# Kernel tuning notes

Measured on AMD Instinct MI355X. Metric: run time of the kernel, lower is better.

Reference implementation:

```python
import jax, jax.numpy as jnp
import numpy as np

B, N, DEG = 64, 512, 16        # graphs, nodes per graph, avg degree
C, HID = 10, 128               # input feat dim (== num_classes quirk), hidden
E = B * N * DEG                # total edges (fixed; pooling masks edges)


def _gcn(x, W, b, src, dst, emask, n):
    # PyG GCNConv: add self-loops, symmetric norm D^-1/2 (A+I) D^-1/2 (XW) + b
    h = x @ W
    deg = jax.ops.segment_sum(emask, dst, num_segments=n) + 1.0  # +1 self-loop
    dinv = jax.lax.rsqrt(deg)
    norm = dinv[src] * dinv[dst] * emask
    agg = jax.ops.segment_sum(h[src] * norm[:, None], dst, num_segments=n)
    return agg + h * (dinv * dinv)[:, None] + b  # self-loop term + bias


def _sag_pool(x, src, dst, emask, Wp, bp, n_per):
    # SAGPooling: score = tanh(GCN(x)); per-graph top-k (ratio=0.5); x' = x[perm]*score
    n = x.shape[0]
    score = jnp.tanh(_gcn(x, Wp, bp, src, dst, emask, n)[:, 0])
    k = n_per // 2
    vals, idx = jax.lax.top_k(score.reshape(B, n_per), k)  # [B,k]
    perm = (idx + (jnp.arange(B) * n_per)[:, None]).reshape(-1)
    xk = x[perm] * vals.reshape(-1)[:, None]
    # relabel edges; drop edges touching removed nodes via mask (fixed E)
    mapping = jnp.full((n,), -1, jnp.int32).at[perm].set(
        jnp.arange(B * k, dtype=jnp.int32))
    ns, nd = mapping[src], mapping[dst]
    nmask = emask * ((ns >= 0) & (nd >= 0)).astype(emask.dtype)
    return xk, jnp.maximum(ns, 0), jnp.maximum(nd, 0), nmask, k


def _readout(x, k):
    # global max pool || global mean pool (all kept nodes are real, no padding)
    xg = x.reshape(B, k, -1)
    return jnp.concatenate([xg.max(axis=1), xg.mean(axis=1)], axis=1)


def setup_inputs() -> dict:
    key = jax.random.key(0)
    ks = jax.random.split(key, 16)
    x = jax.random.normal(ks[0], (B * N, C), jnp.float32)
    off = jnp.repeat(jnp.arange(B, dtype=jnp.int32) * N, N * DEG)
    src = jax.random.randint(ks[1], (E,), 0, N, jnp.int32) + off
    dst = jax.random.randint(ks[2], (E,), 0, N, jnp.int32) + off
    p = lambda k, s: jax.random.normal(k, s, jnp.float32) * 0.05
    return {
        "x": x, "src": src, "dst": dst,
        "W1": p(ks[3], (C, HID)), "b1": jnp.zeros((HID,), jnp.float32),
        "W2": p(ks[4], (HID, HID)), "b2": jnp.zeros((HID,), jnp.float32),
        "W3": p(ks[5], (HID, HID)), "b3": jnp.zeros((HID,), jnp.float32),
        "Wp": p(ks[6], (HID, 1)), "bp": jnp.zeros((1,), jnp.float32),
        "L1W": p(ks[7], (2 * HID, HID)), "L1b": jnp.zeros((HID,), jnp.float32),
        "L2W": p(ks[8], (HID, HID // 2)), "L2b": jnp.zeros((HID // 2,), jnp.float32),
    }


def reference(x, src, dst, W1, b1, W2, b2, W3, b3, Wp, bp, L1W, L1b, L2W, L2b):
    emask = jnp.ones((E,), jnp.float32)
    h = jax.nn.relu(_gcn(x, W1, b1, src, dst, emask, B * N))
    h, src, dst, emask, k = _sag_pool(h, src, dst, emask, Wp, bp, N)
    x1 = _readout(h, k)
    h = jax.nn.relu(_gcn(h, W2, b2, src, dst, emask, B * k))
    h, src, dst, emask, k = _sag_pool(h, src, dst, emask, Wp, bp, k)
    x2 = _readout(h, k)
    h = jax.nn.relu(_gcn(h, W3, b3, src, dst, emask, B * k))
    h, src, dst, emask, k = _sag_pool(h, src, dst, emask, Wp, bp, k)
    x3 = _readout(h, k)
    z = x1 + x2 + x3
    z = jax.nn.relu(z @ L1W + L1b)
    # dropout inactive in eval mode
    z = jax.nn.relu(z @ L2W + L2b)
    return jax.nn.log_softmax(z, axis=1)
```

## Files before the change

### kernel.cpp

```cpp
#include <hip/hip_runtime.h>
#include <math.h>

#define BGR 64
#define N0 512
#define E_TOT (BGR*N0*16)
#define EPG 8192
#define EIT 16
#define HID 128


__global__ __launch_bounds__(512) void k_topo0(
    const int* __restrict__ s0, const int* __restrict__ d0,
    int2* __restrict__ edges, int* __restrict__ cnt, int* __restrict__ rowptr,
    float* __restrict__ dinv, int2* __restrict__ csr){
  __shared__ int   deg[512];
  __shared__ int   cur[512];
  __shared__ float dl[512];
  __shared__ int   wsum[8];
  int g = (blockIdx.x & 7)*8 + (blockIdx.x >> 3);
  int t = threadIdx.x;
  int gbase = g*N0, ebase = g*EPG;
  deg[t] = 0;
  __syncthreads();
  int2 ebuf[EIT];
  #pragma unroll
  for (int it = 0; it < EIT; it++){
    int i = ebase + it*512 + t;
    int2 e = make_int2(s0[i], d0[i]);
    ebuf[it] = e;
    edges[i] = e;
    atomicAdd(&deg[e.y - gbase], 1);
  }
  __syncthreads();
  int vdeg = deg[t];
  int lane = t & 63, wid = t >> 6;
  int x = vdeg;
  #pragma unroll
  for (int off = 1; off < 64; off <<= 1){
    int y = __shfl_up(x, off);
    if (lane >= off) x += y;
  }
  if (lane == 63) wsum[wid] = x;
  __syncthreads();
  int prefix = 0;
  #pragma unroll
  for (int wj = 0; wj < 8; wj++) prefix += (wj < wid) ? wsum[wj] : 0;
  int excl = x + prefix - vdeg;
  rowptr[gbase + t] = ebase + excl;
  cnt[gbase + t] = vdeg;
  cur[t] = excl;
  float dv = rsqrtf((float)vdeg + 1.f);
  dl[t] = dv;
  dinv[gbase + t] = dv;
  __syncthreads();
  #pragma unroll
  for (int it = 0; it < EIT; it++){
    int2 e = ebuf[it];
    int sl = e.x - gbase, dc = e.y - gbase;
    int pos = atomicAdd(&cur[dc], 1);
    csr[ebase + pos] = make_int2(e.x, __float_as_int(dl[sl]*dl[dc]));
  }
}

__global__ __launch_bounds__(512) void k_l1_fused(
    const float* __restrict__ x, const float* __restrict__ W1,
    const int2* __restrict__ csr, const int* __restrict__ rowptr,
    const int* __restrict__ cnt, const float* __restrict__ dinv,
    const float* __restrict__ b1, const float* __restrict__ Wp,
    float4* __restrict__ gout4, float* __restrict__ hp_part){
  extern __shared__ float hl[];
  int b = blockIdx.x;
  int xcd = b & 7, idx = b >> 3;
  int graph = xcd*8 + (idx >> 3);
  int sub = idx & 7;
  int qf = sub >> 1, half = sub & 1;
  int t = threadIdx.x;
  int gbase = graph*N0;
  int fp = t & 31;
  int f = qf*32 + fp;
  float wcol[10];
  #pragma unroll
  for (int k = 0; k < 10; k++) wcol[k] = W1[k*HID + f];
  for (int n = t >> 5; n < N0; n += 16){
    const float* xr = x + (gbase + n)*10;
    float acc = 0.f;
    #pragma unroll
    for (int k = 0; k < 10; k++) acc += xr[k]*wcol[k];
    hl[n*32 + fp] = acc;
  }
  __syncthreads();
  const float4* hl4 = (const float4*)hl;
  int l = t & 7, grp = t >> 3;
  float4 bb = ((const float4*)b1)[qf*8 + l];
  float4 wp = ((const float4*)Wp)[qf*8 + l];
  int n0 = half*256;
  for (int nl = n0 + grp; nl < n0 + 256; nl += 64){
    int node = gbase + nl;
    int start = rowptr[node], c = cnt[node];
    float4 acc = make_float4(0.f,0.f,0.f,0.f);
    int j = 0;
    for (; j + 4 <= c; j += 4){
      int2 e0 = csr[start+j],   e1 = csr[start+j+1];
      int2 e2 = csr[start+j+2], e3 = csr[start+j+3];
      float4 h0 = hl4[(e0.x - gbase)*8 + l];
      float4 h1 = hl4[(e1.x - gbase)*8 + l];
      float4 h2 = hl4[(e2.x - gbase)*8 + l];
      float4 h3 = hl4[(e3.x - gbase)*8 + l];
      float w0 = __int_as_float(e0.y), w1 = __int_as_float(e1.y);
      float w2 = __int_as_float(e2.y), w3 = __int_as_float(e3.y);
      acc.x += w0*h0.x + w1*h1.x + w2*h2.x + w3*h3.x;
      acc.y += w0*h0.y + w1*h1.y + w2*h2.y + w3*h3.y;
      acc.z += w0*h0.z + w1*h1.z + w2*h2.z + w3*h3.z;
      acc.w += w0*h0.w + w1*h1.w + w2*h2.w + w3*h3.w;
    }
    for (; j < c; j++){
      int2 e = csr[start + j];
      float wgt = __int_as_float(e.y);
      float4 hv = hl4[(e.x - gbase)*8 + l];
      acc.x += wgt*hv.x; acc.y += wgt*hv.y; acc.z += wgt*hv.z; acc.w += wgt*hv.w;
    }
    float di = dinv[node], dd = di*di;
    float4 hs = hl4[nl*8 + l];
    float4 v;
    v.x = fmaxf(acc.x + hs.x*dd + bb.x, 0.f);
    v.y = fmaxf(acc.y + hs.y*dd + bb.y, 0.f);
    v.z = fmaxf(acc.z + hs.z*dd + bb.z, 0.f);
    v.w = fmaxf(acc.w + hs.w*dd + bb.w, 0.f);
    gout4[node*32 + qf*8 + l] = v;
    float contrib = v.x*wp.x + v.y*wp.y + v.z*wp.z + v.w*wp.w;
    #pragma unroll
    for (int off = 4; off; off >>= 1) contrib += __shfl_down(contrib, off, 8);
    if (l == 0) hp_part[qf*32768 + node] = contrib;
  }
}

__global__ void k_gemm16p(const float* __restrict__ gprev,
                          const int* __restrict__ sig,
                          const float* __restrict__ svg,
                          const float* __restrict__ W,
                          float* __restrict__ out, int nprev, int nper){
  __shared__ float xr[16][HID];
  int b = blockIdx.x;
  int xcd = b & 7, idx = b >> 3, bpg = nper >> 4;
  int graph = xcd*8 + idx / bpg;
  int lb = (idx % bpg)*16;
  int f = threadIdx.x;
  #pragma unroll
  for (int nd = 0; nd < 16; nd++){
    int row  = sig[graph*512 + lb + nd];
    float val = svg[graph*512 + lb + nd];
    xr[nd][f] = gprev[(graph*nprev + row)*HID + f] * val;
  }
  __syncthreads();
  float acc[16];
  #pragma unroll
  for (int nd = 0; nd < 16; nd++) acc[nd] = 0.f;
  for (int i = 0; i < HID; i++){
    float wv = W[i*HID + f];
    #pragma unroll
    for (int nd = 0; nd < 16; nd++) acc[nd] += xr[nd][i]*wv;
  }
  #pragma unroll
  for (int nd = 0; nd < 16; nd++) out[(graph*nper + lb + nd)*HID + f] = acc[nd];
}

__global__ __launch_bounds__(256) void k_gcn_gather(
    const float4* __restrict__ h4, const int2* __restrict__ csr,
    const int* __restrict__ rowptr, const int* __restrict__ cnt,
    const float* __restrict__ dinv, const float4* __restrict__ bias4,
    const float4* __restrict__ Wp4, float4* __restrict__ out4,
    float* __restrict__ hp, int nper){
  int b = blockIdx.x;
  int xcd = b & 7, idx = b >> 3, bpg = nper >> 3;
  int graph = xcd*8 + idx / bpg;
  int node = graph*nper + (idx % bpg)*8 + (threadIdx.x >> 5);
  int l = threadIdx.x & 31;
  int start = rowptr[node], c = cnt[node];
  float4 acc = make_float4(0.f, 0.f, 0.f, 0.f);
  int j = 0;
  for (; j + 4 <= c; j += 4){
    int2 e0 = csr[start+j],   e1 = csr[start+j+1];
    int2 e2 = csr[start+j+2], e3 = csr[start+j+3];
    float4 h0 = h4[e0.x*32 + l];
    float4 h1 = h4[e1.x*32 + l];
    float4 h2 = h4[e2.x*32 + l];
    float4 h3 = h4[e3.x*32 + l];
    float w0 = __int_as_float(e0.y), w1 = __int_as_float(e1.y);
    float w2 = __int_as_float(e2.y), w3 = __int_as_float(e3.y);
    acc.x += w0*h0.x + w1*h1.x + w2*h2.x + w3*h3.x;
    acc.y += w0*h0.y + w1*h1.y + w2*h2.y + w3*h3.y;
    acc.z += w0*h0.z + w1*h1.z + w2*h2.z + w3*h3.z;
    acc.w += w0*h0.w + w1*h1.w + w2*h2.w + w3*h3.w;
  }
  for (; j < c; j++){
    int2 e = csr[start + j];
    float wgt = __int_as_float(e.y);
    float4 hv = h4[e.x*32 + l];
    acc.x += wgt*hv.x; acc.y += wgt*hv.y; acc.z += wgt*hv.z; acc.w += wgt*hv.w;
  }
  float di = dinv[node], dd = di*di;
  float4 hs = h4[node*32 + l];
  float4 bb = bias4[l];
  float4 v;
  v.x = fmaxf(acc.x + hs.x*dd + bb.x, 0.f);
  v.y = fmaxf(acc.y + hs.y*dd + bb.y, 0.f);
  v.z = fmaxf(acc.z + hs.z*dd + bb.z, 0.f);
  v.w = fmaxf(acc.w + hs.w*dd + bb.w, 0.f);
  out4[node*32 + l] = v;
  float4 wp = Wp4[l];
  float contrib = v.x*wp.x + v.y*wp.y + v.z*wp.z + v.w*wp.w;
  #pragma unroll
  for (int off = 16; off; off >>= 1) contrib += __shfl_down(contrib, off, 32);
  if (l == 0) hp[node] = contrib;
}

__global__ __launch_bounds__(1024) void k_mega(
    const float4* __restrict__ gout4, const float* __restrict__ hp_part,
    int l1flag, const float* __restrict__ hp,
    int2* __restrict__ csr, int* __restrict__ rowptr, int* __restrict__ cnt,
    float* __restrict__ dinv, const float* __restrict__ bp,
    int2* __restrict__ edges, int* __restrict__ sig, float* __restrict__ svg,
    float* __restrict__ z, int nper, int lastlev,
    const float* __restrict__ L1W, const float* __restrict__ L1b,
    const float* __restrict__ L2W, const float* __restrict__ L2b,
    float* __restrict__ out){
  __shared__ float sv[512];
  __shared__ int   si[512];
  __shared__ float hpl[512];
  __shared__ float spart[1024];
  __shared__ int   map_[512];
  __shared__ int   sb[512];
  __shared__ int   cur[256];
  __shared__ float dl[256];
  __shared__ int   wsum[4];
  __shared__ float4 pmx[16][32];
  __shared__ float4 psm[16][32];
  __shared__ float zr[256];
  __shared__ float h1[128];
  __shared__ float h2[64];
  __shared__ float red[2];
  int g = (blockIdx.x & 7)*8 + (blockIdx.x >> 3);
  int t = threadIdx.x;
  int k = nper >> 1;
  int gbase = g*nper, ebase = g*EPG, gb2 = g*k;
  int SPL = 1024/nper;
  int n = t & (nper-1), p = t / nper;
  bool act = t < nper;

  if (act){
    int node = gbase + t;
    hpl[t] = l1flag ? (hp_part[node] + hp_part[32768 + node] +
                       hp_part[65536 + node] + hp_part[98304 + node])
                    : hp[node];
  }
  __syncthreads();
  {
    int start = rowptr[gbase + n], c = cnt[gbase + n];
    int lo = (c*p)/SPL, hi = (c*(p+1))/SPL;
    float a = 0.f;
    for (int j = lo; j < hi; j++){
      int2 e = csr[start + j];
      a += __int_as_float(e.y)*hpl[e.x - gbase];
    }
    spart[t] = a;
  }
  __syncthreads();
  float v = 0.f; int idx = t;
  if (act){
    float a = 0.f;
    for (int pp = 0; pp < SPL; pp++) a += spart[t + pp*nper];
    float di = dinv[gbase + t];
    v = tanhf(a + hpl[t]*di*di + bp[0]);
  }
  for (int kk = 2; kk <= nper; kk <<= 1){
    for (int jj = kk >> 1; jj > 0; jj >>= 1){
      if (jj >= 64){
        if (act){ sv[t] = v; si[t] = idx; }
        __syncthreads();
        if (act){
          int pr = t ^ jj;
          float pv = sv[pr]; int pi = si[pr];
          bool amLower = (t & jj) == 0;
          bool dirDesc = (t & kk) == 0;
          bool betterMine = (v > pv) || (v == pv && idx < pi);
          if ((amLower == dirDesc) != betterMine){ v = pv; idx = pi; }
        }
        __syncthreads();
      } else if (act){
        float pv = __shfl_xor(v, jj);
        int   pi = __shfl_xor(idx, jj);
        bool amLower = (t & jj) == 0;
        bool dirDesc = (t & kk) == 0;
        bool betterMine = (v > pv) || (v == pv && idx < pi);
        if ((amLower == dirDesc) != betterMine){ v = pv; idx = pi; }
      }
    }
  }
  if (act){ sv[t] = v; si[t] = idx; }
  __syncthreads();
  int l = t & 31, j0 = t >> 5;
  if (t < 512){
    float4 mx = make_float4(-INFINITY,-INFINITY,-INFINITY,-INFINITY);
    float4 sm = make_float4(0.f,0.f,0.f,0.f);
    for (int j = j0; j < k; j += 16){
      float val = sv[j]; int row = si[j];
      float4 hv = gout4[(gbase + row)*32 + l];
      float4 o = make_float4(hv.x*val, hv.y*val, hv.z*val, hv.w*val);
      mx.x = fmaxf(mx.x, o.x); mx.y = fmaxf(mx.y, o.y);
      mx.z = fmaxf(mx.z, o.z); mx.w = fmaxf(mx.w, o.w);
      sm.x += o.x; sm.y += o.y; sm.z += o.z; sm.w += o.w;
    }
    pmx[j0][l] = mx; psm[j0][l] = sm;
  }
  if (t < 512 && t < k && !lastlev){ sig[g*512 + t] = si[t]; svg[g*512 + t] = sv[t]; }
  __syncthreads();
  if (t < 32){
    float4 M = pmx[0][t], S = psm[0][t];
    #pragma unroll
    for (int q = 1; q < 16; q++){
      float4 m2 = pmx[q][t], s2 = psm[q][t];
      M.x = fmaxf(M.x, m2.x); M.y = fmaxf(M.y, m2.y);
      M.z = fmaxf(M.z, m2.z); M.w = fmaxf(M.w, m2.w);
      S.x += s2.x; S.y += s2.y; S.z += s2.z; S.w += s2.w;
    }
    float ki = 1.f/(float)k;
    float* zp = z + g*256;
    if (l1flag){
      zp[t*4+0] = M.x; zp[t*4+1] = M.y; zp[t*4+2] = M.z; zp[t*4+3] = M.w;
      zp[128+t*4+0] = S.x*ki; zp[128+t*4+1] = S.y*ki;
      zp[128+t*4+2] = S.z*ki; zp[128+t*4+3] = S.w*ki;
    } else if (!lastlev){
      zp[t*4+0] += M.x; zp[t*4+1] += M.y; zp[t*4+2] += M.z; zp[t*4+3] += M.w;
      zp[128+t*4+0] += S.x*ki; zp[128+t*4+1] += S.y*ki;
      zp[128+t*4+2] += S.z*ki; zp[128+t*4+3] += S.w*ki;
    } else {
      zr[t*4+0] = zp[t*4+0] + M.x; zr[t*4+1] = zp[t*4+1] + M.y;
      zr[t*4+2] = zp[t*4+2] + M.z; zr[t*4+3] = zp[t*4+3] + M.w;
      zr[128+t*4+0] = zp[128+t*4+0] + S.x*ki;
      zr[128+t*4+1] = zp[128+t*4+1] + S.y*ki;
      zr[128+t*4+2] = zp[128+t*4+2] + S.z*ki;
      zr[128+t*4+3] = zp[128+t*4+3] + S.w*ki;
    }
  }
  if (lastlev){
    __syncthreads();
    if (t < 128){
      float a = L1b[t];
      for (int i = 0; i < 256; i++) a += zr[i]*L1W[i*128 + t];
      h1[t] = fmaxf(a, 0.f);
    }
    __syncthreads();
    if (t < 64){
      float a = L2b[t];
      for (int i = 0; i < 128; i++) a += h1[i]*L2W[i*64 + t];
      h2[t] = fmaxf(a, 0.f);
    }
    __syncthreads();
    if (t == 0){
      float mxv = -INFINITY;
      for (int i = 0; i < 64; i++) mxv = fmaxf(mxv, h2[i]);
      float s = 0.f;
      for (int i = 0; i < 64; i++) s += expf(h2[i] - mxv);
      red[0] = mxv; red[1] = logf(s);
    }
    __syncthreads();
    if (t < 64) out[g*64 + t] = h2[t] - red[0] - red[1];
    return;
  }
  if (act) map_[t] = -1;
  if (t < k) sb[t] = 0;
  __syncthreads();
  if (t < k) map_[si[t]] = t;
  __syncthreads();
  int2 ebuf[8];
  #pragma unroll
  for (int it = 0; it < 8; it++){
    int i = ebase + it*1024 + t;
    int2 e = edges[i];
    int2 ne = make_int2(-1, 0);
    if (e.x >= 0){
      int ns = map_[e.x - gbase], nd = map_[e.y - gbase];
      if (ns >= 0 && nd >= 0){
        ne = make_int2(gb2 + ns, gb2 + nd);
        atomicAdd(&sb[nd], 1);
      }
    }
    ebuf[it] = ne;
    edges[i] = ne;
  }
  __syncthreads();
  int vdeg = (t < k) ? sb[t] : 0;
  int lane = t & 63, wid = t >> 6;
  int x = vdeg;
  #pragma unroll
  for (int off = 1; off < 64; off <<= 1){
    int y = __shfl_up(x, off);
    if (lane >= off) x += y;
  }
  if (t < k && lane == 63) wsum[wid] = x;
  __syncthreads();
  if (t < k){
    int prefix = 0;
    #pragma unroll
    for (int wj = 0; wj < 4; wj++) prefix += (wj < wid) ? wsum[wj] : 0;
    int excl = x + prefix - vdeg;
    rowptr[gb2 + t] = ebase + excl;
    cnt[gb2 + t] = vdeg;
    cur[t] = excl;
    float dv = rsqrtf((float)vdeg + 1.f);
    dl[t] = dv;
    dinv[gb2 + t] = dv;
  }
  __syncthreads();
  #pragma unroll
  for (int it = 0; it < 8; it++){
    int2 e = ebuf[it];
    if (e.x >= 0){
      int sl = e.x - gb2, dc = e.y - gb2;
      int pos = atomicAdd(&cur[dc], 1);
      csr[ebase + pos] = make_int2(e.x, __float_as_int(dl[sl]*dl[dc]));
    }
  }
}

extern "C" void kernel_launch(void* const* d_in, const int* in_sizes, int n_in,
                              void* d_out, int out_size, void* d_ws, size_t ws_size,
                              hipStream_t stream){
  (void)in_sizes; (void)n_in; (void)out_size; (void)ws_size;
  const float* x0  = (const float*)d_in[0];
  const int*   s0  = (const int*)  d_in[1];
  const int*   d0  = (const int*)  d_in[2];
  const float* W1  = (const float*)d_in[3];  const float* b1 = (const float*)d_in[4];
  const float* W2  = (const float*)d_in[5];  const float* b2 = (const float*)d_in[6];
  const float* W3  = (const float*)d_in[7];  const float* b3 = (const float*)d_in[8];
  const float* Wp  = (const float*)d_in[9];  const float* bp = (const float*)d_in[10];
  const float* L1W = (const float*)d_in[11]; const float* L1b = (const float*)d_in[12];
  const float* L2W = (const float*)d_in[13]; const float* L2b = (const float*)d_in[14];
  float* out = (float*)d_out;

  float* w = (float*)d_ws;
  float* h     = w; w += 32768*HID;
  float* gout  = w; w += 32768*HID;
  float* dinvv = w; w += 32768;
  float* hp    = w; w += 32768;
  float* hppt  = w; w += 4*32768;
  float* z     = w; w += BGR*256;
  float* svg   = w; w += 32768;
  int* sig     = (int*)w; w += 32768;
  int* cnt     = (int*)w; w += 32768;
  int* rowptr  = (int*)w; w += 32768;
  int2* edges  = (int2*)w; w += 2*E_TOT;
  int2* csr    = (int2*)w; w += 2*E_TOT;

  k_topo0<<<BGR, 512, 0, stream>>>(s0, d0, edges, cnt, rowptr, dinvv, csr);

  k_l1_fused<<<512, 512, 65536, stream>>>(x0, W1, csr, rowptr, cnt, dinvv,
                                          b1, Wp, (float4*)gout, hppt);
  k_mega<<<BGR, 1024, 0, stream>>>((const float4*)gout, hppt, 1, hp, csr,
                                   rowptr, cnt, dinvv, bp, edges, sig, svg,
                                   z, 512, 0, L1W, L1b, L2W, L2b, out);
  k_gemm16p<<<16384/16, HID, 0, stream>>>(gout, sig, svg, W2, h, 512, 256);
  k_gcn_gather<<<16384/8, 256, 0, stream>>>((const float4*)h, csr, rowptr, cnt,
                                            dinvv, (const float4*)b2,
                                            (const float4*)Wp, (float4*)gout,
                                            hp, 256);
  k_mega<<<BGR, 1024, 0, stream>>>((const float4*)gout, hppt, 0, hp, csr,
                                   rowptr, cnt, dinvv, bp, edges, sig, svg,
                                   z, 256, 0, L1W, L1b, L2W, L2b, out);
  k_gemm16p<<<8192/16, HID, 0, stream>>>(gout, sig, svg, W3, h, 256, 128);
  k_gcn_gather<<<8192/8, 256, 0, stream>>>((const float4*)h, csr, rowptr, cnt,
                                           dinvv, (const float4*)b3,
                                           (const float4*)Wp, (float4*)gout,
                                           hp, 128);
  k_mega<<<BGR, 1024, 0, stream>>>((const float4*)gout, hppt, 0, hp, csr,
                                   rowptr, cnt, dinvv, bp, edges, sig, svg,
                                   z, 128, 1, L1W, L1b, L2W, L2b, out);
}
```

Before: 243.0 us.

## Fuse pooling, GEMM and GCN gather into per-level per-graph mega kernels

Replaces the generic mega kernel plus separate gemm16p and gcn_gather launches with three specialized per-graph kernels (megaA/B/C). Each one fuses pooling, the next layer's weight GEMM and the GCN gather into a single 1024-thread block per graph, keeping features in LDS and using per-level CSR offsets. This cuts the launch count from nine to five and removes global round trips. It also swizzles the LDS layout in the layer-1 kernel to reduce bank conflicts. In exchange, each level now runs on only 64 blocks, so parallelism for the GEMM and gather drops sharply.

```diff
diff --git a/kernel.cpp b/kernel.cpp
--- a/kernel.cpp
+++ b/kernel.cpp
@@ -7,7 +7,102 @@
 #define EPG 8192
 #define EIT 16
 #define HID 128
-
+#define LOFF2 32768
+#define LOFF3 49152
+
+#define HSW(r,l) (((r)<<3) | (((l)+(r))&7))
+
+__device__ __forceinline__ void bitonic_sort(float* sv, int* si, float v, int idx,
+                                             int t, int nper, bool act){
+  for (int kk = 2; kk <= nper; kk <<= 1){
+    for (int jj = kk >> 1; jj > 0; jj >>= 1){
+      if (jj >= 64){
+        if (act){ sv[t] = v; si[t] = idx; }
+        __syncthreads();
+        if (act){
+          int p = t ^ jj;
+          float pv = sv[p]; int pi = si[p];
+          bool amLower = (t & jj) == 0;
+          bool dirDesc = (t & kk) == 0;
+          bool betterMine = (v > pv) || (v == pv && idx < pi);
+          if ((amLower == dirDesc) != betterMine){ v = pv; idx = pi; }
+        }
+        __syncthreads();
+      } else if (act){
+        float pv = __shfl_xor(v, jj);
+        int   pi = __shfl_xor(idx, jj);
+        bool amLower = (t & jj) == 0;
+        bool dirDesc = (t & kk) == 0;
+        bool betterMine = (v > pv) || (v == pv && idx < pi);
+        if ((amLower == dirDesc) != betterMine){ v = pv; idx = pi; }
+      }
+    }
+  }
+  if (act){ sv[t] = v; si[t] = idx; }
+  __syncthreads();
+}
+
+__device__ __forceinline__ void relabel1024(
+    int2* __restrict__ edges, int2* __restrict__ csr, const int* si,
+    int* map_, int* sb, int* cur, float* dl, int* wsum,
+    int* __restrict__ rowptr, int* __restrict__ cnt, float* __restrict__ dinv,
+    int t, int nper, int k, int gbase, int gbnew, int ebase, int loff){
+  if (t < nper) map_[t] = -1;
+  if (t < k) sb[t] = 0;
+  __syncthreads();
+  if (t < k) map_[si[t]] = t;
+  __syncthreads();
+  int2 ebuf[8];
+  #pragma unroll
+  for (int it = 0; it < 8; it++){
+    int i = ebase + it*1024 + t;
+    int2 e = edges[i];
+    int2 ne = make_int2(-1, 0);
+    if (e.x >= 0){
+      int ns = map_[e.x - gbase], nd = map_[e.y - gbase];
+      if (ns >= 0 && nd >= 0){
+        ne = make_int2(gbnew + ns, gbnew + nd);
+        atomicAdd(&sb[nd], 1);
+      }
+    }
+    ebuf[it] = ne;
+    edges[i] = ne;
+  }
+  __syncthreads();
+  int vdeg = (t < k) ? sb[t] : 0;
+  int lane = t & 63, wid = t >> 6;
+  int x = vdeg;
+  #pragma unroll
+  for (int off = 1; off < 64; off <<= 1){
+    int y = __shfl_up(x, off);
+    if (lane >= off) x += y;
+  }
+  if (t < k && lane == 63) wsum[wid] = x;
+  __syncthreads();
+  if (t < k){
+    int prefix = 0;
+    #pragma unroll
+    for (int wj = 0; wj < 4; wj++) prefix += (wj < wid) ? wsum[wj] : 0;
+    int excl = x + prefix - vdeg;
+    rowptr[loff + gbnew + t] = ebase + excl;
+    cnt[loff + gbnew + t] = vdeg;
+    cur[t] = excl;
+    float dv = rsqrtf((float)vdeg + 1.f);
+    dl[t] = dv;
+    dinv[loff + gbnew + t] = dv;
+  }
+  __syncthreads();
+  #pragma unroll
+  for (int it = 0; it < 8; it++){
+    int2 e = ebuf[it];
+    if (e.x >= 0){
+      int sl = e.x - gbnew, dc = e.y - gbnew;
+      int pos = atomicAdd(&cur[dc], 1);
+      csr[ebase + pos] = make_int2(e.x, __float_as_int(dl[sl]*dl[dc]));
+    }
+  }
+  __syncthreads();
+}
 
 __global__ __launch_bounds__(512) void k_topo0(
     const int* __restrict__ s0, const int* __restrict__ d0,
@@ -86,7 +181,7 @@
     float acc = 0.f;
     #pragma unroll
     for (int k = 0; k < 10; k++) acc += xr[k]*wcol[k];
-    hl[n*32 + fp] = acc;
+    hl[n*32 + ((((fp>>2)+n)&7)<<2) + (fp&3)] = acc;
   }
   __syncthreads();
   const float4* hl4 = (const float4*)hl;
@@ -102,10 +197,10 @@
     for (; j + 4 <= c; j += 4){
       int2 e0 = csr[start+j],   e1 = csr[start+j+1];
       int2 e2 = csr[start+j+2], e3 = csr[start+j+3];
-      float4 h0 = hl4[(e0.x - gbase)*8 + l];
-      float4 h1 = hl4[(e1.x - gbase)*8 + l];
-      float4 h2 = hl4[(e2.x - gbase)*8 + l];
-      float4 h3 = hl4[(e3.x - gbase)*8 + l];
+      float4 h0 = hl4[HSW(e0.x - gbase, l)];
+      float4 h1 = hl4[HSW(e1.x - gbase, l)];
+      float4 h2 = hl4[HSW(e2.x - gbase, l)];
+      float4 h3 = hl4[HSW(e3.x - gbase, l)];
       float w0 = __int_as_float(e0.y), w1 = __int_as_float(e1.y);
       float w2 = __int_as_float(e2.y), w3 = __int_as_float(e3.y);
       acc.x += w0*h0.x + w1*h1.x + w2*h2.x + w3*h3.x;
@@ -116,11 +211,11 @@
     for (; j < c; j++){
       int2 e = csr[start + j];
       float wgt = __int_as_float(e.y);
-      float4 hv = hl4[(e.x - gbase)*8 + l];
+      float4 hv = hl4[HSW(e.x - gbase, l)];
       acc.x += wgt*hv.x; acc.y += wgt*hv.y; acc.z += wgt*hv.z; acc.w += wgt*hv.w;
     }
     float di = dinv[node], dd = di*di;
-    float4 hs = hl4[nl*8 + l];
+    float4 hs = hl4[HSW(nl, l)];
     float4 v;
     v.x = fmaxf(acc.x + hs.x*dd + bb.x, 0.f);
     v.y = fmaxf(acc.y + hs.y*dd + bb.y, 0.f);
@@ -134,175 +229,57 @@
   }
 }
 
-__global__ void k_gemm16p(const float* __restrict__ gprev,
-                          const int* __restrict__ sig,
-                          const float* __restrict__ svg,
-                          const float* __restrict__ W,
-                          float* __restrict__ out, int nprev, int nper){
-  __shared__ float xr[16][HID];
-  int b = blockIdx.x;
-  int xcd = b & 7, idx = b >> 3, bpg = nper >> 4;
-  int graph = xcd*8 + idx / bpg;
-  int lb = (idx % bpg)*16;
-  int f = threadIdx.x;
-  #pragma unroll
-  for (int nd = 0; nd < 16; nd++){
-    int row  = sig[graph*512 + lb + nd];
-    float val = svg[graph*512 + lb + nd];
-    xr[nd][f] = gprev[(graph*nprev + row)*HID + f] * val;
-  }
-  __syncthreads();
-  float acc[16];
-  #pragma unroll
-  for (int nd = 0; nd < 16; nd++) acc[nd] = 0.f;
-  for (int i = 0; i < HID; i++){
-    float wv = W[i*HID + f];
-    #pragma unroll
-    for (int nd = 0; nd < 16; nd++) acc[nd] += xr[nd][i]*wv;
-  }
-  #pragma unroll
-  for (int nd = 0; nd < 16; nd++) out[(graph*nper + lb + nd)*HID + f] = acc[nd];
-}
-
-__global__ __launch_bounds__(256) void k_gcn_gather(
-    const float4* __restrict__ h4, const int2* __restrict__ csr,
-    const int* __restrict__ rowptr, const int* __restrict__ cnt,
-    const float* __restrict__ dinv, const float4* __restrict__ bias4,
-    const float4* __restrict__ Wp4, float4* __restrict__ out4,
-    float* __restrict__ hp, int nper){
-  int b = blockIdx.x;
-  int xcd = b & 7, idx = b >> 3, bpg = nper >> 3;
-  int graph = xcd*8 + idx / bpg;
-  int node = graph*nper + (idx % bpg)*8 + (threadIdx.x >> 5);
-  int l = threadIdx.x & 31;
-  int start = rowptr[node], c = cnt[node];
-  float4 acc = make_float4(0.f, 0.f, 0.f, 0.f);
-  int j = 0;
-  for (; j + 4 <= c; j += 4){
-    int2 e0 = csr[start+j],   e1 = csr[start+j+1];
-    int2 e2 = csr[start+j+2], e3 = csr[start+j+3];
-    float4 h0 = h4[e0.x*32 + l];
-    float4 h1 = h4[e1.x*32 + l];
-    float4 h2 = h4[e2.x*32 + l];
-    float4 h3 = h4[e3.x*32 + l];
-    float w0 = __int_as_float(e0.y), w1 = __int_as_float(e1.y);
-    float w2 = __int_as_float(e2.y), w3 = __int_as_float(e3.y);
-    acc.x += w0*h0.x + w1*h1.x + w2*h2.x + w3*h3.x;
-    acc.y += w0*h0.y + w1*h1.y + w2*h2.y + w3*h3.y;
-    acc.z += w0*h0.z + w1*h1.z + w2*h2.z + w3*h3.z;
-    acc.w += w0*h0.w + w1*h1.w + w2*h2.w + w3*h3.w;
-  }
-  for (; j < c; j++){
-    int2 e = csr[start + j];
-    float wgt = __int_as_float(e.y);
-    float4 hv = h4[e.x*32 + l];
-    acc.x += wgt*hv.x; acc.y += wgt*hv.y; acc.z += wgt*hv.z; acc.w += wgt*hv.w;
-  }
-  float di = dinv[node], dd = di*di;
-  float4 hs = h4[node*32 + l];
-  float4 bb = bias4[l];
-  float4 v;
-  v.x = fmaxf(acc.x + hs.x*dd + bb.x, 0.f);
-  v.y = fmaxf(acc.y + hs.y*dd + bb.y, 0.f);
-  v.z = fmaxf(acc.z + hs.z*dd + bb.z, 0.f);
-  v.w = fmaxf(acc.w + hs.w*dd + bb.w, 0.f);
-  out4[node*32 + l] = v;
-  float4 wp = Wp4[l];
-  float contrib = v.x*wp.x + v.y*wp.y + v.z*wp.z + v.w*wp.w;
-  #pragma unroll
-  for (int off = 16; off; off >>= 1) contrib += __shfl_down(contrib, off, 32);
-  if (l == 0) hp[node] = contrib;
-}
-
-__global__ __launch_bounds__(1024) void k_mega(
-    const float4* __restrict__ gout4, const float* __restrict__ hp_part,
-    int l1flag, const float* __restrict__ hp,
+__global__ __launch_bounds__(1024) void k_megaA(
+    const float4* __restrict__ gout4, const float* __restrict__ hppt,
     int2* __restrict__ csr, int* __restrict__ rowptr, int* __restrict__ cnt,
     float* __restrict__ dinv, const float* __restrict__ bp,
-    int2* __restrict__ edges, int* __restrict__ sig, float* __restrict__ svg,
-    float* __restrict__ z, int nper, int lastlev,
-    const float* __restrict__ L1W, const float* __restrict__ L1b,
-    const float* __restrict__ L2W, const float* __restrict__ L2b,
-    float* __restrict__ out){
+    int2* __restrict__ edges, const float* __restrict__ W2,
+    float* __restrict__ h2, float* __restrict__ z){
   __shared__ float sv[512];
   __shared__ int   si[512];
   __shared__ float hpl[512];
-  __shared__ float spart[1024];
-  __shared__ int   map_[512];
-  __shared__ int   sb[512];
-  __shared__ int   cur[256];
+  __shared__ union UA {
+    float spart[1024];
+    struct { float4 pmx[16][32]; float4 psm[16][32]; } ro;
+    struct { int map_[512]; int sb[512]; int cur[256]; } rl;
+  } u;
   __shared__ float dl[256];
   __shared__ int   wsum[4];
-  __shared__ float4 pmx[16][32];
-  __shared__ float4 psm[16][32];
-  __shared__ float zr[256];
-  __shared__ float h1[128];
-  __shared__ float h2[64];
-  __shared__ float red[2];
+  __shared__ float xch[64*HID];
   int g = (blockIdx.x & 7)*8 + (blockIdx.x >> 3);
   int t = threadIdx.x;
-  int k = nper >> 1;
-  int gbase = g*nper, ebase = g*EPG, gb2 = g*k;
-  int SPL = 1024/nper;
-  int n = t & (nper-1), p = t / nper;
-  bool act = t < nper;
-
-  if (act){
+  int gbase = g*N0, ebase = g*EPG, gb2 = g*256;
+  float bp0 = bp[0];
+  if (t < 512){
     int node = gbase + t;
-    hpl[t] = l1flag ? (hp_part[node] + hp_part[32768 + node] +
-                       hp_part[65536 + node] + hp_part[98304 + node])
-                    : hp[node];
+    hpl[t] = hppt[node] + hppt[32768+node] + hppt[65536+node] + hppt[98304+node];
   }
   __syncthreads();
   {
+    int n = t & 511, p = t >> 9;
     int start = rowptr[gbase + n], c = cnt[gbase + n];
-    int lo = (c*p)/SPL, hi = (c*(p+1))/SPL;
+    int lo = (c*p) >> 1, hi = (c*(p+1)) >> 1;
     float a = 0.f;
     for (int j = lo; j < hi; j++){
       int2 e = csr[start + j];
       a += __int_as_float(e.y)*hpl[e.x - gbase];
     }
-    spart[t] = a;
+    u.spart[t] = a;
   }
   __syncthreads();
   float v = 0.f; int idx = t;
-  if (act){
-    float a = 0.f;
-    for (int pp = 0; pp < SPL; pp++) a += spart[t + pp*nper];
+  if (t < 512){
+    float a = u.spart[t] + u.spart[t + 512];
     float di = dinv[gbase + t];
-    v = tanhf(a + hpl[t]*di*di + bp[0]);
-  }
-  for (int kk = 2; kk <= nper; kk <<= 1){
-    for (int jj = kk >> 1; jj > 0; jj >>= 1){
-      if (jj >= 64){
-        if (act){ sv[t] = v; si[t] = idx; }
-        __syncthreads();
-        if (act){
-          int pr = t ^ jj;
-          float pv = sv[pr]; int pi = si[pr];
-          bool amLower = (t & jj) == 0;
-          bool dirDesc = (t & kk) == 0;
-          bool betterMine = (v > pv) || (v == pv && idx < pi);
-          if ((amLower == dirDesc) != betterMine){ v = pv; idx = pi; }
-        }
-        __syncthreads();
-      } else if (act){
-        float pv = __shfl_xor(v, jj);
-        int   pi = __shfl_xor(idx, jj);
-        bool amLower = (t & jj) == 0;
-        bool dirDesc = (t & kk) == 0;
-        bool betterMine = (v > pv) || (v == pv && idx < pi);
-        if ((amLower == dirDesc) != betterMine){ v = pv; idx = pi; }
-      }
-    }
-  }
-  if (act){ sv[t] = v; si[t] = idx; }
-  __syncthreads();
+    v = tanhf(a + hpl[t]*di*di + bp0);
+  }
+  __syncthreads();
+  bitonic_sort(sv, si, v, idx, t, 512, t < 512);
   int l = t & 31, j0 = t >> 5;
   if (t < 512){
     float4 mx = make_float4(-INFINITY,-INFINITY,-INFINITY,-INFINITY);
     float4 sm = make_float4(0.f,0.f,0.f,0.f);
-    for (int j = j0; j < k; j += 16){
+    for (int j = j0; j < 256; j += 16){
       float val = sv[j]; int row = si[j];
       float4 hv = gout4[(gbase + row)*32 + l];
       float4 o = make_float4(hv.x*val, hv.y*val, hv.z*val, hv.w*val);
@@ -310,117 +287,348 @@
       mx.z = fmaxf(mx.z, o.z); mx.w = fmaxf(mx.w, o.w);
       sm.x += o.x; sm.y += o.y; sm.z += o.z; sm.w += o.w;
     }
-    pmx[j0][l] = mx; psm[j0][l] = sm;
-  }
-  if (t < 512 && t < k && !lastlev){ sig[g*512 + t] = si[t]; svg[g*512 + t] = sv[t]; }
+    u.ro.pmx[j0][l] = mx; u.ro.psm[j0][l] = sm;
+  }
   __syncthreads();
   if (t < 32){
-    float4 M = pmx[0][t], S = psm[0][t];
+    float4 M = u.ro.pmx[0][t], S = u.ro.psm[0][t];
     #pragma unroll
     for (int q = 1; q < 16; q++){
-      float4 m2 = pmx[q][t], s2 = psm[q][t];
+      float4 m2 = u.ro.pmx[q][t], s2 = u.ro.psm[q][t];
       M.x = fmaxf(M.x, m2.x); M.y = fmaxf(M.y, m2.y);
       M.z = fmaxf(M.z, m2.z); M.w = fmaxf(M.w, m2.w);
       S.x += s2.x; S.y += s2.y; S.z += s2.z; S.w += s2.w;
     }
-    float ki = 1.f/(float)k;
+    float ki = 1.f/256.f;
     float* zp = z + g*256;
-    if (l1flag){
-      zp[t*4+0] = M.x; zp[t*4+1] = M.y; zp[t*4+2] = M.z; zp[t*4+3] = M.w;
-      zp[128+t*4+0] = S.x*ki; zp[128+t*4+1] = S.y*ki;
-      zp[128+t*4+2] = S.z*ki; zp[128+t*4+3] = S.w*ki;
-    } else if (!lastlev){
-      zp[t*4+0] += M.x; zp[t*4+1] += M.y; zp[t*4+2] += M.z; zp[t*4+3] += M.w;
-      zp[128+t*4+0] += S.x*ki; zp[128+t*4+1] += S.y*ki;
-      zp[128+t*4+2] += S.z*ki; zp[128+t*4+3] += S.w*ki;
-    } else {
-      zr[t*4+0] = zp[t*4+0] + M.x; zr[t*4+1] = zp[t*4+1] + M.y;
-      zr[t*4+2] = zp[t*4+2] + M.z; zr[t*4+3] = zp[t*4+3] + M.w;
-      zr[128+t*4+0] = zp[128+t*4+0] + S.x*ki;
-      zr[128+t*4+1] = zp[128+t*4+1] + S.y*ki;
-      zr[128+t*4+2] = zp[128+t*4+2] + S.z*ki;
-      zr[128+t*4+3] = zp[128+t*4+3] + S.w*ki;
-    }
-  }
-  if (lastlev){
+    zp[t*4+0] = M.x; zp[t*4+1] = M.y; zp[t*4+2] = M.z; zp[t*4+3] = M.w;
+    zp[128+t*4+0] = S.x*ki; zp[128+t*4+1] = S.y*ki;
+    zp[128+t*4+2] = S.z*ki; zp[128+t*4+3] = S.w*ki;
+  }
+  __syncthreads();
+  relabel1024(edges, csr, si, u.rl.map_, u.rl.sb, u.rl.cur, dl, wsum,
+              rowptr, cnt, dinv, t, 512, 256, gbase, gb2, ebase, LOFF2);
+  for (int c0 = 0; c0 < 256; c0 += 64){
+    {
+      int r = c0 + (t >> 4);
+      int f0 = (t & 15) * 8;
+      float val = sv[r]; int row = si[r];
+      const float4* src = (const float4*)((const float*)gout4 +
+                                          (gbase + row)*HID + f0);
+      float4 a0 = src[0], a1 = src[1];
+      float4* dst = (float4*)(xch + (t>>4)*HID + f0);
+      dst[0] = make_float4(a0.x*val, a0.y*val, a0.z*val, a0.w*val);
+      dst[1] = make_float4(a1.x*val, a1.y*val, a1.z*val, a1.w*val);
+    }
     __syncthreads();
-    if (t < 128){
-      float a = L1b[t];
-      for (int i = 0; i < 256; i++) a += zr[i]*L1W[i*128 + t];
-      h1[t] = fmaxf(a, 0.f);
+    {
+      int f = t & 127, ng = t >> 7;
+      float acc[8];
+      #pragma unroll
+      for (int q = 0; q < 8; q++) acc[q] = 0.f;
+      for (int i = 0; i < HID; i++){
+        float wv = W2[i*HID + f];
+        #pragma unroll
+        for (int q = 0; q < 8; q++) acc[q] += xch[(ng*8+q)*HID + i]*wv;
+      }
+      #pragma unroll
+      for (int q = 0; q < 8; q++)
+        h2[(gb2 + c0 + ng*8 + q)*HID + f] = acc[q];
     }
     __syncthreads();
-    if (t < 64){
-      float a = L2b[t];
-      for (int i = 0; i < 128; i++) a += h1[i]*L2W[i*64 + t];
-      h2[t] = fmaxf(a, 0.f);
-    }
-    __syncthreads();
-    if (t == 0){
-      float mxv = -INFINITY;
-      for (int i = 0; i < 64; i++) mxv = fmaxf(mxv, h2[i]);
-      float s = 0.f;
-      for (int i = 0; i < 64; i++) s += expf(h2[i] - mxv);
-      red[0] = mxv; red[1] = logf(s);
-    }
-    __syncthreads();
-    if (t < 64) out[g*64 + t] = h2[t] - red[0] - red[1];
-    return;
-  }
-  if (act) map_[t] = -1;
-  if (t < k) sb[t] = 0;
-  __syncthreads();
-  if (t < k) map_[si[t]] = t;
-  __syncthreads();
-  int2 ebuf[8];
-  #pragma unroll
-  for (int it = 0; it < 8; it++){
-    int i = ebase + it*1024 + t;
-    int2 e = edges[i];
-    int2 ne = make_int2(-1, 0);
-    if (e.x >= 0){
-      int ns = map_[e.x - gbase], nd = map_[e.y - gbase];
-      if (ns >= 0 && nd >= 0){
-        ne = make_int2(gb2 + ns, gb2 + nd);
-        atomicAdd(&sb[nd], 1);
+  }
+}
+
+__global__ __launch_bounds__(1024) void k_megaB(
+    const float* __restrict__ h2, int2* __restrict__ csr,
+    int* __restrict__ rowptr, int* __restrict__ cnt, float* __restrict__ dinv,
+    const float* __restrict__ bp, int2* __restrict__ edges,
+    const float* __restrict__ b2, const float* __restrict__ Wp,
+    const float* __restrict__ W3, float* __restrict__ h3,
+    float* __restrict__ z){
+  __shared__ float gl[256*HID];
+  __shared__ float sv[256];
+  __shared__ int   si[256];
+  __shared__ float hpl[256];
+  __shared__ union UB {
+    float spart[1024];
+    struct { float4 pmx[16][32]; float4 psm[16][32]; } ro;
+    struct { int map_[256]; int sb[128]; int cur[128]; } rl;
+  } u;
+  __shared__ float dl[128];
+  __shared__ int   wsum[4];
+  int g = (blockIdx.x & 7)*8 + (blockIdx.x >> 3);
+  int t = threadIdx.x;
+  int gb2 = g*256, gb3 = g*128, ebase = g*EPG;
+  const float4* h24 = (const float4*)h2;
+  float4* gl4 = (float4*)gl;
+  int l = t & 31, r0 = t >> 5;
+  float bp0 = bp[0];
+  {
+    float4 bb = ((const float4*)b2)[l];
+    float4 wp = ((const float4*)Wp)[l];
+    for (int it = 0; it < 8; it++){
+      int n = it*32 + r0;
+      int node = gb2 + n;
+      int start = rowptr[LOFF2 + node], c = cnt[LOFF2 + node];
+      float4 acc = make_float4(0.f,0.f,0.f,0.f);
+      int j = 0;
+      for (; j + 4 <= c; j += 4){
+        int2 e0 = csr[start+j],   e1 = csr[start+j+1];
+        int2 e2 = csr[start+j+2], e3 = csr[start+j+3];
+        float4 h0 = h24[e0.x*32 + l];
+        float4 h1 = h24[e1.x*32 + l];
+        float4 hq2 = h24[e2.x*32 + l];
+        float4 hq3 = h24[e3.x*32 + l];
+        float w0 = __int_as_float(e0.y), w1 = __int_as_float(e1.y);
+        float w2 = __int_as_float(e2.y), w3 = __int_as_float(e3.y);
+        acc.x += w0*h0.x + w1*h1.x + w2*hq2.x + w3*hq3.x;
+        acc.y += w0*h0.y + w1*h1.y + w2*hq2.y + w3*hq3.y;
+        acc.z += w0*h0.z + w1*h1.z + w2*hq2.z + w3*hq3.z;
+        acc.w += w0*h0.w + w1*h1.w + w2*hq2.w + w3*hq3.w;
       }
-    }
-    ebuf[it] = ne;
-    edges[i] = ne;
-  }
-  __syncthreads();
-  int vdeg = (t < k) ? sb[t] : 0;
-  int lane = t & 63, wid = t >> 6;
-  int x = vdeg;
-  #pragma unroll
-  for (int off = 1; off < 64; off <<= 1){
-    int y = __shfl_up(x, off);
-    if (lane >= off) x += y;
-  }
-  if (t < k && lane == 63) wsum[wid] = x;
-  __syncthreads();
-  if (t < k){
-    int prefix = 0;
-    #pragma unroll
-    for (int wj = 0; wj < 4; wj++) prefix += (wj < wid) ? wsum[wj] : 0;
-    int excl = x + prefix - vdeg;
-    rowptr[gb2 + t] = ebase + excl;
-    cnt[gb2 + t] = vdeg;
-    cur[t] = excl;
-    float dv = rsqrtf((float)vdeg + 1.f);
-    dl[t] = dv;
-    dinv[gb2 + t] = dv;
-  }
-  __syncthreads();
-  #pragma unroll
-  for (int it = 0; it < 8; it++){
-    int2 e = ebuf[it];
-    if (e.x >= 0){
-      int sl = e.x - gb2, dc = e.y - gb2;
-      int pos = atomicAdd(&cur[dc], 1);
-      csr[ebase + pos] = make_int2(e.x, __float_as_int(dl[sl]*dl[dc]));
-    }
-  }
+      for (; j < c; j++){
+        int2 e = csr[start + j];
+        float wgt = __int_as_float(e.y);
+        float4 hv = h24[e.x*32 + l];
+        acc.x += wgt*hv.x; acc.y += wgt*hv.y; acc.z += wgt*hv.z; acc.w += wgt*hv.w;
+      }
+      float di = dinv[LOFF2 + node], dd = di*di;
+      float4 hs = h24[node*32 + l];
+      float4 v;
+      v.x = fmaxf(acc.x + hs.x*dd + bb.x, 0.f);
+      v.y = fmaxf(acc.y + hs.y*dd + bb.y, 0.f);
+      v.z = fmaxf(acc.z + hs.z*dd + bb.z, 0.f);
+      v.w = fmaxf(acc.w + hs.w*dd + bb.w, 0.f);
+      gl4[n*32 + l] = v;
+      float contrib = v.x*wp.x + v.y*wp.y + v.z*wp.z + v.w*wp.w;
+      #pragma unroll
+      for (int off = 16; off; off >>= 1) contrib += __shfl_down(contrib, off, 32);
+      if (l == 0) hpl[n] = contrib;
+    }
+  }
+  __syncthreads();
+  {
+    int n = t & 255, p = t >> 8;
+    int start = rowptr[LOFF2 + gb2 + n], c = cnt[LOFF2 + gb2 + n];
+    int lo = (c*p) >> 2, hi = (c*(p+1)) >> 2;
+    float a = 0.f;
+    for (int j = lo; j < hi; j++){
+      int2 e = csr[start + j];
+      a += __int_as_float(e.y)*hpl[e.x - gb2];
+    }
+    u.spart[t] = a;
+  }
+  __syncthreads();
+  float v = 0.f; int idx = t;
+  if (t < 256){
+    float a = u.spart[t] + u.spart[t+256] + u.spart[t+512] + u.spart[t+768];
+    float di = dinv[LOFF2 + gb2 + t];
+    v = tanhf(a + hpl[t]*di*di + bp0);
+  }
+  __syncthreads();
+  bitonic_sort(sv, si, v, idx, t, 256, t < 256);
+  int j0 = t >> 5;
+  if (t < 512){
+    float4 mx = make_float4(-INFINITY,-INFINITY,-INFINITY,-INFINITY);
+    float4 sm = make_float4(0.f,0.f,0.f,0.f);
+    for (int j = j0; j < 128; j += 16){
+      float val = sv[j]; int row = si[j];
+      float4 hv = gl4[row*32 + l];
+      float4 o = make_float4(hv.x*val, hv.y*val, hv.z*val, hv.w*val);
+      mx.x = fmaxf(mx.x, o.x); mx.y = fmaxf(mx.y, o.y);
+      mx.z = fmaxf(mx.z, o.z); mx.w = fmaxf(mx.w, o.w);
+      sm.x += o.x; sm.y += o.y; sm.z += o.z; sm.w += o.w;
+    }
+    u.ro.pmx[j0][l] = mx; u.ro.psm[j0][l] = sm;
+  }
+  __syncthreads();
+  if (t < 32){
+    float4 M = u.ro.pmx[0][t], S = u.ro.psm[0][t];
+    #pragma unroll
+    for (int q = 1; q < 16; q++){
+      float4 m2 = u.ro.pmx[q][t], s2 = u.ro.psm[q][t];
+      M.x = fmaxf(M.x, m2.x); M.y = fmaxf(M.y, m2.y);
+      M.z = fmaxf(M.z, m2.z); M.w = fmaxf(M.w, m2.w);
+      S.x += s2.x; S.y += s2.y; S.z += s2.z; S.w += s2.w;
+    }
+    float ki = 1.f/128.f;
+    float* zp = z + g*256;
+    zp[t*4+0] += M.x; zp[t*4+1] += M.y; zp[t*4+2] += M.z; zp[t*4+3] += M.w;
+    zp[128+t*4+0] += S.x*ki; zp[128+t*4+1] += S.y*ki;
+    zp[128+t*4+2] += S.z*ki; zp[128+t*4+3] += S.w*ki;
+  }
+  __syncthreads();
+  relabel1024(edges, csr, si, u.rl.map_, u.rl.sb, u.rl.cur, dl, wsum,
+              rowptr, cnt, dinv, t, 256, 128, gb2, gb3, ebase, LOFF3);
+  {
+    int f = t & 127, ng = t >> 7;
+    int ri[16]; float vv[16];
+    #pragma unroll
+    for (int q = 0; q < 16; q++){ ri[q] = si[ng*16+q]; vv[q] = sv[ng*16+q]; }
+    float acc[16];
+    #pragma unroll
+    for (int q = 0; q < 16; q++) acc[q] = 0.f;
+    for (int i = 0; i < HID; i++){
+      float wv = W3[i*HID + f];
+      #pragma unroll
+      for (int q = 0; q < 16; q++) acc[q] += (gl[ri[q]*HID + i]*vv[q])*wv;
+    }
+    #pragma unroll
+    for (int q = 0; q < 16; q++)
+      h3[(gb3 + ng*16 + q)*HID + f] = acc[q];
+  }
+}
+
+__global__ __launch_bounds__(1024) void k_megaC(
+    const float* __restrict__ h3, const int2* __restrict__ csr,
+    const int* __restrict__ rowptr, const int* __restrict__ cnt,
+    const float* __restrict__ dinv, const float* __restrict__ bp,
+    const float* __restrict__ b3, const float* __restrict__ Wp,
+    float* __restrict__ z,
+    const float* __restrict__ L1W, const float* __restrict__ L1b,
+    const float* __restrict__ L2W, const float* __restrict__ L2b,
+    float* __restrict__ out){
+  __shared__ float gl[128*HID];
+  __shared__ float sv[128];
+  __shared__ int   si[128];
+  __shared__ float hpl[128];
+  __shared__ union UC {
+    float spart[1024];
+    struct { float4 pmx[16][32]; float4 psm[16][32]; } ro;
+  } u;
+  __shared__ float zr[256];
+  __shared__ float h1l[128];
+  __shared__ float h2l[64];
+  __shared__ float red[2];
+  int g = (blockIdx.x & 7)*8 + (blockIdx.x >> 3);
+  int t = threadIdx.x;
+  int gb3 = g*128;
+  const float4* h34 = (const float4*)h3;
+  float4* gl4 = (float4*)gl;
+  int l = t & 31, r0 = t >> 5;
+  float bp0 = bp[0];
+  {
+    float4 bb = ((const float4*)b3)[l];
+    float4 wp = ((const float4*)Wp)[l];
+    for (int it = 0; it < 4; it++){
+      int n = it*32 + r0;
+      int node = gb3 + n;
+      int start = rowptr[LOFF3 + node], c = cnt[LOFF3 + node];
+      float4 acc = make_float4(0.f,0.f,0.f,0.f);
+      int j = 0;
+      for (; j + 4 <= c; j += 4){
+        int2 e0 = csr[start+j],   e1 = csr[start+j+1];
+        int2 e2 = csr[start+j+2], e3 = csr[start+j+3];
+        float4 h0 = h34[e0.x*32 + l];
+        float4 h1 = h34[e1.x*32 + l];
+        float4 hq2 = h34[e2.x*32 + l];
+        float4 hq3 = h34[e3.x*32 + l];
+        float w0 = __int_as_float(e0.y), w1 = __int_as_float(e1.y);
+        float w2 = __int_as_float(e2.y), w3 = __int_as_float(e3.y);
+        acc.x += w0*h0.x + w1*h1.x + w2*hq2.x + w3*hq3.x;
+        acc.y += w0*h0.y + w1*h1.y + w2*hq2.y + w3*hq3.y;
+        acc.z += w0*h0.z + w1*h1.z + w2*hq2.z + w3*hq3.z;
+        acc.w += w0*h0.w + w1*h1.w + w2*hq2.w + w3*hq3.w;
+      }
+      for (; j < c; j++){
+        int2 e = csr[start + j];
+        float wgt = __int_as_float(e.y);
+        float4 hv = h34[e.x*32 + l];
+        acc.x += wgt*hv.x; acc.y += wgt*hv.y; acc.z += wgt*hv.z; acc.w += wgt*hv.w;
+      }
+      float di = dinv[LOFF3 + node], dd = di*di;
+      float4 hs = h34[node*32 + l];
+      float4 v;
+      v.x = fmaxf(acc.x + hs.x*dd + bb.x, 0.f);
+      v.y = fmaxf(acc.y + hs.y*dd + bb.y, 0.f);
+      v.z = fmaxf(acc.z + hs.z*dd + bb.z, 0.f);
+      v.w = fmaxf(acc.w + hs.w*dd + bb.w, 0.f);
+      gl4[n*32 + l] = v;
+      float contrib = v.x*wp.x + v.y*wp.y + v.z*wp.z + v.w*wp.w;
+      #pragma unroll
+      for (int off = 16; off; off >>= 1) contrib += __shfl_down(contrib, off, 32);
+      if (l == 0) hpl[n] = contrib;
+    }
+  }
+  __syncthreads();
+  {
+    int n = t & 127, p = t >> 7;
+    int start = rowptr[LOFF3 + gb3 + n], c = cnt[LOFF3 + gb3 + n];
+    int lo = (c*p) >> 3, hi = (c*(p+1)) >> 3;
+    float a = 0.f;
+    for (int j = lo; j < hi; j++){
+      int2 e = csr[start + j];
+      a += __int_as_float(e.y)*hpl[e.x - gb3];
+    }
+    u.spart[t] = a;
+  }
+  __syncthreads();
+  float v = 0.f; int idx = t;
+  if (t < 128){
+    float a = 0.f;
+    #pragma unroll
+    for (int pp = 0; pp < 8; pp++) a += u.spart[t + pp*128];
+    float di = dinv[LOFF3 + gb3 + t];
+    v = tanhf(a + hpl[t]*di*di + bp0);
+  }
+  __syncthreads();
+  bitonic_sort(sv, si, v, idx, t, 128, t < 128);
+  int j0 = t >> 5;
+  if (t < 512){
+    float4 mx = make_float4(-INFINITY,-INFINITY,-INFINITY,-INFINITY);
+    float4 sm = make_float4(0.f,0.f,0.f,0.f);
+    for (int j = j0; j < 64; j += 16){
+      float val = sv[j]; int row = si[j];
+      float4 hv = gl4[row*32 + l];
+      float4 o = make_float4(hv.x*val, hv.y*val, hv.z*val, hv.w*val);
+      mx.x = fmaxf(mx.x, o.x); mx.y = fmaxf(mx.y, o.y);
+      mx.z = fmaxf(mx.z, o.z); mx.w = fmaxf(mx.w, o.w);
+      sm.x += o.x; sm.y += o.y; sm.z += o.z; sm.w += o.w;
+    }
+    u.ro.pmx[j0][l] = mx; u.ro.psm[j0][l] = sm;
+  }
+  __syncthreads();
+  if (t < 32){
+    float4 M = u.ro.pmx[0][t], S = u.ro.psm[0][t];
+    #pragma unroll
+    for (int q = 1; q < 16; q++){
+      float4 m2 = u.ro.pmx[q][t], s2 = u.ro.psm[q][t];
+      M.x = fmaxf(M.x, m2.x); M.y = fmaxf(M.y, m2.y);
+      M.z = fmaxf(M.z, m2.z); M.w = fmaxf(M.w, m2.w);
+      S.x += s2.x; S.y += s2.y; S.z += s2.z; S.w += s2.w;
+    }
+    float ki = 1.f/64.f;
+    float* zp = z + g*256;
+    zr[t*4+0] = zp[t*4+0] + M.x; zr[t*4+1] = zp[t*4+1] + M.y;
+    zr[t*4+2] = zp[t*4+2] + M.z; zr[t*4+3] = zp[t*4+3] + M.w;
+    zr[128+t*4+0] = zp[128+t*4+0] + S.x*ki;
+    zr[128+t*4+1] = zp[128+t*4+1] + S.y*ki;
+    zr[128+t*4+2] = zp[128+t*4+2] + S.z*ki;
+    zr[128+t*4+3] = zp[128+t*4+3] + S.w*ki;
+  }
+  __syncthreads();
+  if (t < 128){
+    float a = L1b[t];
+    for (int i = 0; i < 256; i++) a += zr[i]*L1W[i*128 + t];
+    h1l[t] = fmaxf(a, 0.f);
+  }
+  __syncthreads();
+  if (t < 64){
+    float a = L2b[t];
+    for (int i = 0; i < 128; i++) a += h1l[i]*L2W[i*64 + t];
+    h2l[t] = fmaxf(a, 0.f);
+  }
+  __syncthreads();
+  if (t == 0){
+    float mxv = -INFINITY;
+    for (int i = 0; i < 64; i++) mxv = fmaxf(mxv, h2l[i]);
+    float s = 0.f;
+    for (int i = 0; i < 64; i++) s += expf(h2l[i] - mxv);
+    red[0] = mxv; red[1] = logf(s);
+  }
+  __syncthreads();
+  if (t < 64) out[g*64 + t] = h2l[t] - red[0] - red[1];
 }
 
 extern "C" void kernel_launch(void* const* d_in, const int* in_sizes, int n_in,
@@ -439,40 +647,24 @@
   float* out = (float*)d_out;
 
   float* w = (float*)d_ws;
-  float* h     = w; w += 32768*HID;
   float* gout  = w; w += 32768*HID;
-  float* dinvv = w; w += 32768;
-  float* hp    = w; w += 32768;
+  float* h2    = w; w += 16384*HID;
+  float* h3    = w; w += 8192*HID;
+  float* dinvv = w; w += 65536;
   float* hppt  = w; w += 4*32768;
   float* z     = w; w += BGR*256;
-  float* svg   = w; w += 32768;
-  int* sig     = (int*)w; w += 32768;
-  int* cnt     = (int*)w; w += 32768;
-  int* rowptr  = (int*)w; w += 32768;
+  int* cnt     = (int*)w; w += 65536;
+  int* rowptr  = (int*)w; w += 65536;
   int2* edges  = (int2*)w; w += 2*E_TOT;
   int2* csr    = (int2*)w; w += 2*E_TOT;
 
   k_topo0<<<BGR, 512, 0, stream>>>(s0, d0, edges, cnt, rowptr, dinvv, csr);
-
   k_l1_fused<<<512, 512, 65536, stream>>>(x0, W1, csr, rowptr, cnt, dinvv,
                                           b1, Wp, (float4*)gout, hppt);
-  k_mega<<<BGR, 1024, 0, stream>>>((const float4*)gout, hppt, 1, hp, csr,
-                                   rowptr, cnt, dinvv, bp, edges, sig, svg,
-                                   z, 512, 0, L1W, L1b, L2W, L2b, out);
-  k_gemm16p<<<16384/16, HID, 0, stream>>>(gout, sig, svg, W2, h, 512, 256);
-  k_gcn_gather<<<16384/8, 256, 0, stream>>>((const float4*)h, csr, rowptr, cnt,
-                                            dinvv, (const float4*)b2,
-                                            (const float4*)Wp, (float4*)gout,
-                                            hp, 256);
-  k_mega<<<BGR, 1024, 0, stream>>>((const float4*)gout, hppt, 0, hp, csr,
-                                   rowptr, cnt, dinvv, bp, edges, sig, svg,
-                                   z, 256, 0, L1W, L1b, L2W, L2b, out);
-  k_gemm16p<<<8192/16, HID, 0, stream>>>(gout, sig, svg, W3, h, 256, 128);
-  k_gcn_gather<<<8192/8, 256, 0, stream>>>((const float4*)h, csr, rowptr, cnt,
-                                           dinvv, (const float4*)b3,
-                                           (const float4*)Wp, (float4*)gout,
-                                           hp, 128);
-  k_mega<<<BGR, 1024, 0, stream>>>((const float4*)gout, hppt, 0, hp, csr,
-                                   rowptr, cnt, dinvv, bp, edges, sig, svg,
-                                   z, 128, 1, L1W, L1b, L2W, L2b, out);
-}
+  k_megaA<<<BGR, 1024, 0, stream>>>((const float4*)gout, hppt, csr, rowptr,
+                                    cnt, dinvv, bp, edges, W2, h2, z);
+  k_megaB<<<BGR, 1024, 0, stream>>>(h2, csr, rowptr, cnt, dinvv, bp, edges,
+                                    b2, Wp, W3, h3, z);
+  k_megaC<<<BGR, 1024, 0, stream>>>(h3, csr, rowptr, cnt, dinvv, bp, b3, Wp,
+                                    z, L1W, L1b, L2W, L2b, out);
+}
```

Result: slower. 296.0 us (+21.8%).
